# Kernel tuning notes

Measured on AMD Instinct MI355X. Metric: run time of the kernel, lower is better.

The kernel has to match this reference:

```python
import jax, jax.numpy as jnp
import numpy as np

B, T, V, E, H, FC, O = 4096, 64, 512, 32, 128, 256, 1024


def setup_inputs() -> dict:
    key = jax.random.key(0)
    ks = jax.random.split(key, 12)
    n = lambda k, shape, sc=1.0: (jax.random.normal(k, shape, jnp.float32) * sc)
    return {
        "message": n(ks[0], (B, T, V), 0.1),
        "W_emb": n(ks[1], (E, V), 0.05),
        "b_emb": n(ks[2], (E,), 0.05),
        "init_emb": n(ks[3], (1, 1, E), 1.0),
        "W_ih": n(ks[4], (3 * H, E), 0.08),
        "W_hh": n(ks[5], (3 * H, H), 0.08),
        "b_ih": n(ks[6], (3 * H,), 0.05),
        "b_hh": n(ks[7], (3 * H,), 0.05),
        "W_fc1": n(ks[8], (FC, H), 0.08),
        "b_fc1": n(ks[9], (FC,), 0.05),
        "W_fc2": n(ks[10], (O, FC), 0.05),
        "b_fc2": n(ks[11], (O,), 0.05),
    }


def reference(message, W_emb, b_emb, init_emb, W_ih, W_hh, b_ih, b_hh,
              W_fc1, b_fc1, W_fc2, b_fc2):
    Bb, Tt, Vv = message.shape
    Hh = W_hh.shape[1]
    # Per-step embedding of the message (torch does this inside the loop;
    # it is a pure per-timestep linear so we batch it once): [B,T,E]
    emb = jnp.einsum('btv,ev->bte', message, W_emb) + b_emb
    # Inputs consumed by the GRU at step t: initial_embedding at t=0,
    # then embedding(message[:, t-1]) for t >= 1. The embedding of the
    # final token is computed in torch but never fed to the GRU.
    x0 = jnp.broadcast_to(init_emb[0], (Bb, init_emb.shape[-1]))  # [B,E]
    xs = jnp.concatenate([x0[:, None, :], emb[:, :Tt - 1, :]], axis=1)  # [B,T,E]
    # Precompute input-side gate pre-activations for all steps: [T,B,3H]
    gi_all = jnp.einsum('bte,ge->tbg', xs, W_ih) + b_ih

    def gru_step(h, gi):
        gh = h @ W_hh.T + b_hh  # [B,3H]
        i_r, i_z, i_n = jnp.split(gi, 3, axis=-1)
        h_r, h_z, h_n = jnp.split(gh, 3, axis=-1)
        r = jax.nn.sigmoid(i_r + h_r)
        z = jax.nn.sigmoid(i_z + h_z)
        nng = jnp.tanh(i_n + r * h_n)
        h_new = (1.0 - z) * nng + z * h
        return h_new, None

    h0 = jnp.zeros((Bb, Hh), message.dtype)
    h_last, _ = jax.lax.scan(gru_step, h0, gi_all)
    hid = jax.nn.elu(h_last @ W_fc1.T + b_fc1)
    return jax.nn.sigmoid(hid @ W_fc2.T + b_fc2)
```

## Files before the change

### kernel.cpp

```cpp
#include <hip/hip_runtime.h>
#include <math.h>

#define B_ 4096
#define T_ 64
#define V_ 512
#define E_ 32
#define H_ 128
#define FC1_ 256
#define O_ 1024

typedef float f32x4 __attribute__((ext_vector_type(4)));
typedef short s16x8 __attribute__((ext_vector_type(8)));
typedef unsigned short u16;

#define MFMA16(a, b, c) __builtin_amdgcn_mfma_f32_16x16x32_bf16(a, b, c, 0, 0, 0)

#define LDS_BARRIER() do {                                   \
    asm volatile("s_waitcnt lgkmcnt(0)" ::: "memory");       \
    __builtin_amdgcn_s_barrier();                            \
} while (0)

union Frag { u16 q[8]; unsigned u[4]; s16x8 v; };

__device__ __forceinline__ u16 f2bf(float f) {
    union { float f; unsigned u; } v; v.f = f;
    unsigned r = v.u + 0x7FFFu + ((v.u >> 16) & 1u);
    return (u16)(r >> 16);
}
__device__ __forceinline__ unsigned cvtpk(float lo, float hi) {
    unsigned r;
    asm("v_cvt_pk_bf16_f32 %0, %1, %2" : "=v"(r) : "v"(lo), "v"(hi));
    return r;
}
__device__ __forceinline__ float sigf(float x) { return 1.0f / (1.0f + __expf(-x)); }
__device__ __forceinline__ float tanhfast(float x) {
    return 1.0f - 2.0f / (__expf(2.0f * x) + 1.0f);
}

__global__ void __launch_bounds__(256) prep_kernel(
    const float* __restrict__ Wih, const float* __restrict__ Whh,
    const float* __restrict__ Wemb, const float* __restrict__ Wfc1,
    const float* __restrict__ Wfc2,
    u16* __restrict__ wihF, u16* __restrict__ whhF, u16* __restrict__ wembF,
    u16* __restrict__ wfc1F, u16* __restrict__ wfc2F) {
    int id = blockIdx.x * 256 + threadIdx.x;
    int np = gridDim.x * 256;
    for (int i = id; i < 24 * 4 * 64 * 8; i += np) {
        int j = i & 7, l = (i >> 3) & 63, kc = (i >> 9) & 3, gt = i >> 11;
        whhF[i] = f2bf(Whh[(gt * 16 + (l & 15)) * 128 + kc * 32 + (l >> 4) * 8 + j]);
    }
    for (int i = id; i < 24 * 64 * 8; i += np) {
        int j = i & 7, l = (i >> 3) & 63, gt = i >> 9;
        wihF[i] = f2bf(Wih[(gt * 16 + (l & 15)) * 32 + (l >> 4) * 8 + j]);
    }
    for (int i = id; i < 2 * 16 * 64 * 8; i += np) {
        int j = i & 7, l = (i >> 3) & 63, kc = (i >> 9) & 15, nt = i >> 13;
        wembF[i] = f2bf(Wemb[(nt * 16 + (l & 15)) * 512 + kc * 32 + (l >> 4) * 8 + j]);
    }
    for (int i = id; i < 16 * 4 * 64 * 8; i += np) {
        int j = i & 7, l = (i >> 3) & 63, kc = (i >> 9) & 3, ot = i >> 11;
        wfc1F[i] = f2bf(Wfc1[(ot * 16 + (l & 15)) * 128 + kc * 32 + (l >> 4) * 8 + j]);
    }
    for (int i = id; i < 64 * 8 * 64 * 8; i += np) {
        int j = i & 7, l = (i >> 3) & 63, kc = (i >> 9) & 7, nt = i >> 12;
        wfc2F[i] = f2bf(Wfc2[(nt * 16 + (l & 15)) * 256 + kc * 32 + (l >> 4) * 8 + j]);
    }
}

__global__ void __launch_bounds__(512, 2) fused_kernel(
    const float* __restrict__ msg,
    const u16* __restrict__ whhF8, const u16* __restrict__ wihF8,
    const u16* __restrict__ wembF8,
    const float* __restrict__ b_ih, const float* __restrict__ b_hh,
    const float* __restrict__ b_emb, const float* __restrict__ init_emb,
    const u16* __restrict__ wfc1F8, const float* __restrict__ b_fc1,
    const u16* __restrict__ wfc2F8, const float* __restrict__ b_fc2,
    float* __restrict__ out) {
    __shared__ u16 hlds[2][16 * 136];
    __shared__ float epart[2][8][576];
    __shared__ u16 xfrag[2][640];
    __shared__ u16 hidl[16 * 264];
    const int tid = threadIdx.x, w = tid >> 6, l = tid & 63;
    const int ln = l & 15, lh = l >> 4;
    const int wg = w & 3, wp = w >> 2;
    const int gb = blockIdx.x;

    for (int i = tid; i < 16 * 136; i += 512) hlds[0][i] = 0;

    const s16x8* whhFv = (const s16x8*)whhF8;
    const s16x8* wihFv = (const s16x8*)wihF8;
    const s16x8* wembFv = (const s16x8*)wembF8;
    s16x8 wh[3][4], wi[3], we[2][2];
    float br, bz, bin, bgn;
    {
        #pragma unroll
        for (int g = 0; g < 3; g++) {
            int gt = wg + 4 * wp + 8 * g;
            #pragma unroll
            for (int kc = 0; kc < 4; kc++) wh[g][kc] = whhFv[(gt * 4 + kc) * 64 + l];
            wi[g] = wihFv[gt * 64 + l];
        }
        int c = wg * 16 + wp * 64 + ln;
        br  = b_ih[c] + b_hh[c];
        bz  = b_ih[128 + c] + b_hh[128 + c];
        bin = b_ih[256 + c];
        bgn = b_hh[256 + c];
        #pragma unroll
        for (int kk = 0; kk < 2; kk++) {
            we[kk][0] = wembFv[(2 * w + kk) * 64 + l];
            we[kk][1] = wembFv[(16 + 2 * w + kk) * 64 + l];
        }
    }
    const float bev = b_emb[tid & 31];

    s16x8 xinit;
    {
        Frag xi;
        #pragma unroll
        for (int j = 0; j < 8; j++) xi.q[j] = f2bf(init_emb[lh * 8 + j]);
        xinit = xi.v;
    }
    float hold[4] = {};
    const float* mrow = msg + (size_t)(gb * 16 + ln) * T_ * V_ + (2 * w) * 32 + lh * 8;
    f32x4 mb0[4], mb1[4], mb2[4], mb3[4];
#define LOADCOL(BUF, C) do {                                   \
    const float* p_ = mrow + (size_t)(C) * 512;                \
    BUF[0] = *(const f32x4*)(p_);                              \
    BUF[1] = *(const f32x4*)(p_ + 4);                          \
    BUF[2] = *(const f32x4*)(p_ + 32);                         \
    BUF[3] = *(const f32x4*)(p_ + 36);                         \
} while (0)

#define EMBED_STORE(MC, PAR) do {                               \
    f32x4 e0 = {0.f, 0.f, 0.f, 0.f}, e1 = {0.f, 0.f, 0.f, 0.f}; \
    _Pragma("unroll")                                           \
    for (int kk = 0; kk < 2; kk++) {                            \
        Frag fa;                                                \
        fa.u[0] = cvtpk(MC[2 * kk][0], MC[2 * kk][1]);          \
        fa.u[1] = cvtpk(MC[2 * kk][2], MC[2 * kk][3]);          \
        fa.u[2] = cvtpk(MC[2 * kk + 1][0], MC[2 * kk + 1][1]);  \
        fa.u[3] = cvtpk(MC[2 * kk + 1][2], MC[2 * kk + 1][3]);  \
        e0 = MFMA16(fa.v, we[kk][0], e0);                       \
        e1 = MFMA16(fa.v, we[kk][1], e1);                       \
    }                                                           \
    _Pragma("unroll")                                           \
    for (int i = 0; i < 4; i++) {                               \
        epart[PAR][w][(lh * 4 + i) * 36 + ln]      = e0[i];     \
        epart[PAR][w][(lh * 4 + i) * 36 + 16 + ln] = e1[i];     \
    }                                                           \
} while (0)

    LOADCOL(mb3, 0);
    EMBED_STORE(mb3, 1);
    LOADCOL(mb0, 1); LOADCOL(mb1, 2); LOADCOL(mb2, 3);
    LDS_BARRIER();

    const int aoff = ln * 136 + lh * 8;
    const int colo = wg * 16 + wp * 64 + ln;
    const int fr = tid >> 5, fc = tid & 31, fo = fr * 36 + fc;

#define GRU_STEP(TT, MC, MN) do {                                              \
    const int t = (TT);                                                        \
    if (t <= 58) LOADCOL(MN, t + 4);                                           \
    const u16* hb = hlds[t & 1];                                               \
    s16x8 af0 = *(const s16x8*)(hb + aoff);                                    \
    s16x8 af1 = *(const s16x8*)(hb + aoff + 32);                               \
    s16x8 af2 = *(const s16x8*)(hb + aoff + 64);                               \
    s16x8 af3 = *(const s16x8*)(hb + aoff + 96);                               \
    s16x8 xc;                                                                  \
    if (t == 0) xc = xinit;                                                    \
    else xc = *(const s16x8*)(&xfrag[(t + 1) & 1][0] + ln * 40 + lh * 8);      \
    f32x4 ar  = {br, br, br, br};                                              \
    f32x4 az  = {bz, bz, bz, bz};                                              \
    f32x4 agn = {bgn, bgn, bgn, bgn};                                          \
    f32x4 ain = {bin, bin, bin, bin};                                          \
    ar  = MFMA16(xc, wi[0], ar);                                               \
    az  = MFMA16(xc, wi[1], az);                                               \
    ain = MFMA16(xc, wi[2], ain);                                              \
    ar  = MFMA16(af0, wh[0][0], ar);                                           \
    ar  = MFMA16(af1, wh[0][1], ar);                                           \
    ar  = MFMA16(af2, wh[0][2], ar);                                           \
    ar  = MFMA16(af3, wh[0][3], ar);                                           \
    az  = MFMA16(af0, wh[1][0], az);                                           \
    az  = MFMA16(af1, wh[1][1], az);                                           \
    az  = MFMA16(af2, wh[1][2], az);                                           \
    az  = MFMA16(af3, wh[1][3], az);                                           \
    agn = MFMA16(af0, wh[2][0], agn);                                          \
    agn = MFMA16(af1, wh[2][1], agn);                                          \
    agn = MFMA16(af2, wh[2][2], agn);                                          \
    agn = MFMA16(af3, wh[2][3], agn);                                          \
    u16* hw = hlds[(t + 1) & 1];                                               \
    float hn[4];                                                               \
    _Pragma("unroll")                                                          \
    for (int i = 0; i < 4; i++) {                                              \
        float rg = sigf(ar[i]);                                                \
        float zg = sigf(az[i]);                                                \
        float ng = tanhfast(ain[i] + rg * agn[i]);                             \
        hn[i] = zg * (hold[i] - ng) + ng;                                      \
        hold[i] = hn[i];                                                       \
    }                                                                          \
    {                                                                          \
        unsigned u01 = cvtpk(hn[0], hn[1]);                                    \
        unsigned u23 = cvtpk(hn[2], hn[3]);                                    \
        hw[(lh * 4 + 0) * 136 + colo] = (u16)(u01 & 0xFFFFu);                  \
        hw[(lh * 4 + 1) * 136 + colo] = (u16)(u01 >> 16);                      \
        hw[(lh * 4 + 2) * 136 + colo] = (u16)(u23 & 0xFFFFu);                  \
        hw[(lh * 4 + 3) * 136 + colo] = (u16)(u23 >> 16);                      \
    }                                                                          \
    if (t <= 61) EMBED_STORE(MC, t & 1);                                       \
    if (t <= 62) {                                                             \
        const float* eb = &epart[(t + 1) & 1][0][0];                           \
        float s = eb[fo]            + eb[576 + fo]     + eb[2 * 576 + fo]      \
                + eb[3 * 576 + fo]  + eb[4 * 576 + fo] + eb[5 * 576 + fo]      \
                + eb[6 * 576 + fo]  + eb[7 * 576 + fo] + bev;                  \
        xfrag[t & 1][fr * 40 + fc] = f2bf(s);                                  \
    }                                                                          \
    LDS_BARRIER();                                                             \
} while (0)

    for (int tt = 0; tt < 64; tt += 4) {
        GRU_STEP(tt + 0, mb0, mb3);
        GRU_STEP(tt + 1, mb1, mb0);
        GRU_STEP(tt + 2, mb2, mb1);
        GRU_STEP(tt + 3, mb3, mb2);
    }
#undef GRU_STEP
#undef LOADCOL
#undef EMBED_STORE

    const u16* hb = hlds[0];
    s16x8 hf0 = *(const s16x8*)(hb + aoff);
    s16x8 hf1 = *(const s16x8*)(hb + aoff + 32);
    s16x8 hf2 = *(const s16x8*)(hb + aoff + 64);
    s16x8 hf3 = *(const s16x8*)(hb + aoff + 96);
    const s16x8* w1v = (const s16x8*)wfc1F8;
    #pragma unroll
    for (int q = 0; q < 2; q++) {
        int ot = 2 * w + q;
        float b1 = b_fc1[ot * 16 + ln];
        f32x4 a1 = {b1, b1, b1, b1};
        a1 = MFMA16(hf0, w1v[(ot * 4 + 0) * 64 + l], a1);
        a1 = MFMA16(hf1, w1v[(ot * 4 + 1) * 64 + l], a1);
        a1 = MFMA16(hf2, w1v[(ot * 4 + 2) * 64 + l], a1);
        a1 = MFMA16(hf3, w1v[(ot * 4 + 3) * 64 + l], a1);
        #pragma unroll
        for (int i = 0; i < 4; i++) {
            float v = a1[i];
            v = v > 0.0f ? v : (__expf(v) - 1.0f);
            hidl[(lh * 4 + i) * 264 + ot * 16 + ln] = f2bf(v);
        }
    }
    LDS_BARRIER();

    s16x8 hf[8];
    #pragma unroll
    for (int kc = 0; kc < 8; kc++)
        hf[kc] = *(const s16x8*)(hidl + ln * 264 + kc * 32 + lh * 8);
    const s16x8* w2v = (const s16x8*)wfc2F8;
    #pragma unroll
    for (int q = 0; q < 8; q++) {
        int nt = 8 * w + q;
        float b2 = b_fc2[nt * 16 + ln];
        f32x4 a2 = {b2, b2, b2, b2};
        #pragma unroll
        for (int kc = 0; kc < 8; kc++)
            a2 = MFMA16(hf[kc], w2v[(nt * 8 + kc) * 64 + l], a2);
        #pragma unroll
        for (int i = 0; i < 4; i++)
            out[(size_t)(gb * 16 + lh * 4 + i) * 1024 + nt * 16 + ln] = sigf(a2[i]);
    }
}

extern "C" void kernel_launch(void* const* d_in, const int* in_sizes, int n_in,
                              void* d_out, int out_size, void* d_ws, size_t ws_size,
                              hipStream_t stream) {
    const float* message  = (const float*)d_in[0];
    const float* W_emb    = (const float*)d_in[1];
    const float* b_emb    = (const float*)d_in[2];
    const float* init_emb = (const float*)d_in[3];
    const float* W_ih     = (const float*)d_in[4];
    const float* W_hh     = (const float*)d_in[5];
    const float* b_ih     = (const float*)d_in[6];
    const float* b_hh     = (const float*)d_in[7];
    const float* W_fc1    = (const float*)d_in[8];
    const float* b_fc1    = (const float*)d_in[9];
    const float* W_fc2    = (const float*)d_in[10];
    const float* b_fc2    = (const float*)d_in[11];
    float* out = (float*)d_out;

    u16* whhF  = (u16*)d_ws;
    u16* wihF  = whhF  + 49152;
    u16* wembF = wihF  + 12288;
    u16* wfc1F = wembF + 16384;
    u16* wfc2F = wfc1F + 32768;

    hipLaunchKernelGGL(prep_kernel, dim3(256), dim3(256), 0, stream,
                       W_ih, W_hh, W_emb, W_fc1, W_fc2, wihF, whhF, wembF, wfc1F, wfc2F);
    hipLaunchKernelGGL(fused_kernel, dim3(256), dim3(512), 0, stream,
                       message, whhF, wihF, wembF, b_ih, b_hh, b_emb, init_emb,
                       wfc1F, b_fc1, wfc2F, b_fc2, out);
}
```

Baseline: 132.2 us.

## Drop weight prep kernel and stream message tiles via global_load_lds

Removes the separate prep kernel that repacked the weights into bf16 fragment layouts. The fused kernel now gathers and converts fp32 weights directly from global memory. Message columns are no longer prefetched into registers four steps ahead; they are double-buffered in LDS with asynchronous global_load_lds, two steps ahead. This saves a kernel launch and frees registers, at the cost of more LDS (about 66KB extra for mlds, which may limit occupancy at 2 blocks/CU), uncoalesced fp32 weight loads in the fc2 epilogue, and a shorter prefetch distance.

Measured after the change: 158.1 us. 1.2x slower.

```diff
diff --git a/kernel.cpp b/kernel.cpp
--- a/kernel.cpp
+++ b/kernel.cpp
@@ -15,11 +15,6 @@
 
 #define MFMA16(a, b, c) __builtin_amdgcn_mfma_f32_16x16x32_bf16(a, b, c, 0, 0, 0)
 
-#define LDS_BARRIER() do {                                   \
-    asm volatile("s_waitcnt lgkmcnt(0)" ::: "memory");       \
-    __builtin_amdgcn_s_barrier();                            \
-} while (0)
-
 union Frag { u16 q[8]; unsigned u[4]; s16x8 v; };
 
 __device__ __forceinline__ u16 f2bf(float f) {
@@ -36,46 +31,32 @@
 __device__ __forceinline__ float tanhfast(float x) {
     return 1.0f - 2.0f / (__expf(2.0f * x) + 1.0f);
 }
-
-__global__ void __launch_bounds__(256) prep_kernel(
-    const float* __restrict__ Wih, const float* __restrict__ Whh,
-    const float* __restrict__ Wemb, const float* __restrict__ Wfc1,
-    const float* __restrict__ Wfc2,
-    u16* __restrict__ wihF, u16* __restrict__ whhF, u16* __restrict__ wembF,
-    u16* __restrict__ wfc1F, u16* __restrict__ wfc2F) {
-    int id = blockIdx.x * 256 + threadIdx.x;
-    int np = gridDim.x * 256;
-    for (int i = id; i < 24 * 4 * 64 * 8; i += np) {
-        int j = i & 7, l = (i >> 3) & 63, kc = (i >> 9) & 3, gt = i >> 11;
-        whhF[i] = f2bf(Whh[(gt * 16 + (l & 15)) * 128 + kc * 32 + (l >> 4) * 8 + j]);
-    }
-    for (int i = id; i < 24 * 64 * 8; i += np) {
-        int j = i & 7, l = (i >> 3) & 63, gt = i >> 9;
-        wihF[i] = f2bf(Wih[(gt * 16 + (l & 15)) * 32 + (l >> 4) * 8 + j]);
-    }
-    for (int i = id; i < 2 * 16 * 64 * 8; i += np) {
-        int j = i & 7, l = (i >> 3) & 63, kc = (i >> 9) & 15, nt = i >> 13;
-        wembF[i] = f2bf(Wemb[(nt * 16 + (l & 15)) * 512 + kc * 32 + (l >> 4) * 8 + j]);
-    }
-    for (int i = id; i < 16 * 4 * 64 * 8; i += np) {
-        int j = i & 7, l = (i >> 3) & 63, kc = (i >> 9) & 3, ot = i >> 11;
-        wfc1F[i] = f2bf(Wfc1[(ot * 16 + (l & 15)) * 128 + kc * 32 + (l >> 4) * 8 + j]);
-    }
-    for (int i = id; i < 64 * 8 * 64 * 8; i += np) {
-        int j = i & 7, l = (i >> 3) & 63, kc = (i >> 9) & 7, nt = i >> 12;
-        wfc2F[i] = f2bf(Wfc2[(nt * 16 + (l & 15)) * 256 + kc * 32 + (l >> 4) * 8 + j]);
-    }
+__device__ __forceinline__ void gll16(const float* gsrc, float* ldst) {
+    __builtin_amdgcn_global_load_lds(
+        (const __attribute__((address_space(1))) unsigned int*)gsrc,
+        (__attribute__((address_space(3))) unsigned int*)ldst,
+        16, 0, 0);
+}
+__device__ __forceinline__ s16x8 gatherB(const float* W, int row, int K, int k0, int lh) {
+    const float* p = W + (size_t)row * K + k0 + lh * 8;
+    float4 a = *(const float4*)p;
+    float4 b = *(const float4*)(p + 4);
+    Frag f;
+    f.u[0] = cvtpk(a.x, a.y); f.u[1] = cvtpk(a.z, a.w);
+    f.u[2] = cvtpk(b.x, b.y); f.u[3] = cvtpk(b.z, b.w);
+    return f.v;
 }
 
 __global__ void __launch_bounds__(512, 2) fused_kernel(
     const float* __restrict__ msg,
-    const u16* __restrict__ whhF8, const u16* __restrict__ wihF8,
-    const u16* __restrict__ wembF8,
+    const float* __restrict__ Wemb, const float* __restrict__ b_emb,
+    const float* __restrict__ init_emb,
+    const float* __restrict__ Wih, const float* __restrict__ Whh,
     const float* __restrict__ b_ih, const float* __restrict__ b_hh,
-    const float* __restrict__ b_emb, const float* __restrict__ init_emb,
-    const u16* __restrict__ wfc1F8, const float* __restrict__ b_fc1,
-    const u16* __restrict__ wfc2F8, const float* __restrict__ b_fc2,
+    const float* __restrict__ Wfc1, const float* __restrict__ b_fc1,
+    const float* __restrict__ Wfc2, const float* __restrict__ b_fc2,
     float* __restrict__ out) {
+    __shared__ float mlds[2][16][516];
     __shared__ u16 hlds[2][16 * 136];
     __shared__ float epart[2][8][576];
     __shared__ u16 xfrag[2][640];
@@ -87,9 +68,19 @@
 
     for (int i = tid; i < 16 * 136; i += 512) hlds[0][i] = 0;
 
-    const s16x8* whhFv = (const s16x8*)whhF8;
-    const s16x8* wihFv = (const s16x8*)wihF8;
-    const s16x8* wembFv = (const s16x8*)wembF8;
+#define GLL_COL(C, BUF) do {                                                   \
+    _Pragma("unroll")                                                          \
+    for (int i_ = 0; i_ < 4; i_++) {                                           \
+        int r_ = 2 * w + (i_ >> 1);                                            \
+        int h_ = (i_ & 1) * 256;                                               \
+        gll16(msg + ((size_t)(gb * 16 + r_) * T_ + (C)) * V_ + h_ + l * 4,     \
+              &mlds[BUF][r_][h_]);                                             \
+    }                                                                          \
+} while (0)
+
+    GLL_COL(0, 0);
+    GLL_COL(1, 1);
+
     s16x8 wh[3][4], wi[3], we[2][2];
     float br, bz, bin, bgn;
     {
@@ -97,22 +88,22 @@
         for (int g = 0; g < 3; g++) {
             int gt = wg + 4 * wp + 8 * g;
             #pragma unroll
-            for (int kc = 0; kc < 4; kc++) wh[g][kc] = whhFv[(gt * 4 + kc) * 64 + l];
-            wi[g] = wihFv[gt * 64 + l];
+            for (int kc = 0; kc < 4; kc++)
+                wh[g][kc] = gatherB(Whh, gt * 16 + ln, 128, kc * 32, lh);
+            wi[g] = gatherB(Wih, gt * 16 + ln, 32, 0, lh);
+        }
+        #pragma unroll
+        for (int kk = 0; kk < 2; kk++) {
+            we[kk][0] = gatherB(Wemb, ln, 512, (2 * w + kk) * 32, lh);
+            we[kk][1] = gatherB(Wemb, 16 + ln, 512, (2 * w + kk) * 32, lh);
         }
         int c = wg * 16 + wp * 64 + ln;
         br  = b_ih[c] + b_hh[c];
         bz  = b_ih[128 + c] + b_hh[128 + c];
         bin = b_ih[256 + c];
         bgn = b_hh[256 + c];
-        #pragma unroll
-        for (int kk = 0; kk < 2; kk++) {
-            we[kk][0] = wembFv[(2 * w + kk) * 64 + l];
-            we[kk][1] = wembFv[(16 + 2 * w + kk) * 64 + l];
-        }
     }
     const float bev = b_emb[tid & 31];
-
     s16x8 xinit;
     {
         Frag xi;
@@ -121,47 +112,38 @@
         xinit = xi.v;
     }
     float hold[4] = {};
-    const float* mrow = msg + (size_t)(gb * 16 + ln) * T_ * V_ + (2 * w) * 32 + lh * 8;
-    f32x4 mb0[4], mb1[4], mb2[4], mb3[4];
-#define LOADCOL(BUF, C) do {                                   \
-    const float* p_ = mrow + (size_t)(C) * 512;                \
-    BUF[0] = *(const f32x4*)(p_);                              \
-    BUF[1] = *(const f32x4*)(p_ + 4);                          \
-    BUF[2] = *(const f32x4*)(p_ + 32);                         \
-    BUF[3] = *(const f32x4*)(p_ + 36);                         \
+    __syncthreads();
+
+#define EMBED_LDS(BUF, PAR) do {                                               \
+    f32x4 e0 = {0.f, 0.f, 0.f, 0.f}, e1 = {0.f, 0.f, 0.f, 0.f};                \
+    _Pragma("unroll")                                                          \
+    for (int kk = 0; kk < 2; kk++) {                                           \
+        const float* mp = &mlds[BUF][ln][(2 * w + kk) * 32 + lh * 8];          \
+        f32x4 m0 = *(const f32x4*)mp;                                          \
+        f32x4 m1 = *(const f32x4*)(mp + 4);                                    \
+        Frag fa;                                                               \
+        fa.u[0] = cvtpk(m0[0], m0[1]); fa.u[1] = cvtpk(m0[2], m0[3]);          \
+        fa.u[2] = cvtpk(m1[0], m1[1]); fa.u[3] = cvtpk(m1[2], m1[3]);          \
+        e0 = MFMA16(fa.v, we[kk][0], e0);                                      \
+        e1 = MFMA16(fa.v, we[kk][1], e1);                                      \
+    }                                                                          \
+    _Pragma("unroll")                                                          \
+    for (int i = 0; i < 4; i++) {                                              \
+        epart[PAR][w][(lh * 4 + i) * 36 + ln]      = e0[i];                    \
+        epart[PAR][w][(lh * 4 + i) * 36 + 16 + ln] = e1[i];                    \
+    }                                                                          \
 } while (0)
 
-#define EMBED_STORE(MC, PAR) do {                               \
-    f32x4 e0 = {0.f, 0.f, 0.f, 0.f}, e1 = {0.f, 0.f, 0.f, 0.f}; \
-    _Pragma("unroll")                                           \
-    for (int kk = 0; kk < 2; kk++) {                            \
-        Frag fa;                                                \
-        fa.u[0] = cvtpk(MC[2 * kk][0], MC[2 * kk][1]);          \
-        fa.u[1] = cvtpk(MC[2 * kk][2], MC[2 * kk][3]);          \
-        fa.u[2] = cvtpk(MC[2 * kk + 1][0], MC[2 * kk + 1][1]);  \
-        fa.u[3] = cvtpk(MC[2 * kk + 1][2], MC[2 * kk + 1][3]);  \
-        e0 = MFMA16(fa.v, we[kk][0], e0);                       \
-        e1 = MFMA16(fa.v, we[kk][1], e1);                       \
-    }                                                           \
-    _Pragma("unroll")                                           \
-    for (int i = 0; i < 4; i++) {                               \
-        epart[PAR][w][(lh * 4 + i) * 36 + ln]      = e0[i];     \
-        epart[PAR][w][(lh * 4 + i) * 36 + 16 + ln] = e1[i];     \
-    }                                                           \
-} while (0)
-
-    LOADCOL(mb3, 0);
-    EMBED_STORE(mb3, 1);
-    LOADCOL(mb0, 1); LOADCOL(mb1, 2); LOADCOL(mb2, 3);
-    LDS_BARRIER();
+    EMBED_LDS(0, 1);
+    __syncthreads();
 
     const int aoff = ln * 136 + lh * 8;
     const int colo = wg * 16 + wp * 64 + ln;
     const int fr = tid >> 5, fc = tid & 31, fo = fr * 36 + fc;
 
-#define GRU_STEP(TT, MC, MN) do {                                              \
+#define GRU_STEP(TT) do {                                                      \
     const int t = (TT);                                                        \
-    if (t <= 58) LOADCOL(MN, t + 4);                                           \
+    if (t <= 60) GLL_COL(t + 2, t & 1);                                        \
     const u16* hb = hlds[t & 1];                                               \
     s16x8 af0 = *(const s16x8*)(hb + aoff);                                    \
     s16x8 af1 = *(const s16x8*)(hb + aoff + 32);                               \
@@ -207,42 +189,39 @@
         hw[(lh * 4 + 2) * 136 + colo] = (u16)(u23 & 0xFFFFu);                  \
         hw[(lh * 4 + 3) * 136 + colo] = (u16)(u23 >> 16);                      \
     }                                                                          \
-    if (t <= 61) EMBED_STORE(MC, t & 1);                                       \
+    if (t <= 61) EMBED_LDS((t + 1) & 1, t & 1);                                \
     if (t <= 62) {                                                             \
         const float* eb = &epart[(t + 1) & 1][0][0];                           \
-        float s = eb[fo]            + eb[576 + fo]     + eb[2 * 576 + fo]      \
-                + eb[3 * 576 + fo]  + eb[4 * 576 + fo] + eb[5 * 576 + fo]      \
-                + eb[6 * 576 + fo]  + eb[7 * 576 + fo] + bev;                  \
+        float s = eb[fo]           + eb[576 + fo]     + eb[2 * 576 + fo]       \
+                + eb[3 * 576 + fo] + eb[4 * 576 + fo] + eb[5 * 576 + fo]       \
+                + eb[6 * 576 + fo] + eb[7 * 576 + fo] + bev;                   \
         xfrag[t & 1][fr * 40 + fc] = f2bf(s);                                  \
     }                                                                          \
-    LDS_BARRIER();                                                             \
+    __syncthreads();                                                           \
 } while (0)
 
-    for (int tt = 0; tt < 64; tt += 4) {
-        GRU_STEP(tt + 0, mb0, mb3);
-        GRU_STEP(tt + 1, mb1, mb0);
-        GRU_STEP(tt + 2, mb2, mb1);
-        GRU_STEP(tt + 3, mb3, mb2);
+    for (int tt = 0; tt < 64; tt += 2) {
+        GRU_STEP(tt);
+        GRU_STEP(tt + 1);
     }
 #undef GRU_STEP
-#undef LOADCOL
-#undef EMBED_STORE
+#undef GLL_COL
+#undef EMBED_LDS
 
     const u16* hb = hlds[0];
     s16x8 hf0 = *(const s16x8*)(hb + aoff);
     s16x8 hf1 = *(const s16x8*)(hb + aoff + 32);
     s16x8 hf2 = *(const s16x8*)(hb + aoff + 64);
     s16x8 hf3 = *(const s16x8*)(hb + aoff + 96);
-    const s16x8* w1v = (const s16x8*)wfc1F8;
     #pragma unroll
     for (int q = 0; q < 2; q++) {
         int ot = 2 * w + q;
         float b1 = b_fc1[ot * 16 + ln];
         f32x4 a1 = {b1, b1, b1, b1};
-        a1 = MFMA16(hf0, w1v[(ot * 4 + 0) * 64 + l], a1);
-        a1 = MFMA16(hf1, w1v[(ot * 4 + 1) * 64 + l], a1);
-        a1 = MFMA16(hf2, w1v[(ot * 4 + 2) * 64 + l], a1);
-        a1 = MFMA16(hf3, w1v[(ot * 4 + 3) * 64 + l], a1);
+        a1 = MFMA16(hf0, gatherB(Wfc1, ot * 16 + ln, 128, 0,  lh), a1);
+        a1 = MFMA16(hf1, gatherB(Wfc1, ot * 16 + ln, 128, 32, lh), a1);
+        a1 = MFMA16(hf2, gatherB(Wfc1, ot * 16 + ln, 128, 64, lh), a1);
+        a1 = MFMA16(hf3, gatherB(Wfc1, ot * 16 + ln, 128, 96, lh), a1);
         #pragma unroll
         for (int i = 0; i < 4; i++) {
             float v = a1[i];
@@ -250,13 +229,12 @@
             hidl[(lh * 4 + i) * 264 + ot * 16 + ln] = f2bf(v);
         }
     }
-    LDS_BARRIER();
+    __syncthreads();
 
     s16x8 hf[8];
     #pragma unroll
     for (int kc = 0; kc < 8; kc++)
         hf[kc] = *(const s16x8*)(hidl + ln * 264 + kc * 32 + lh * 8);
-    const s16x8* w2v = (const s16x8*)wfc2F8;
     #pragma unroll
     for (int q = 0; q < 8; q++) {
         int nt = 8 * w + q;
@@ -264,7 +242,7 @@
         f32x4 a2 = {b2, b2, b2, b2};
         #pragma unroll
         for (int kc = 0; kc < 8; kc++)
-            a2 = MFMA16(hf[kc], w2v[(nt * 8 + kc) * 64 + l], a2);
+            a2 = MFMA16(hf[kc], gatherB(Wfc2, nt * 16 + ln, 256, kc * 32, lh), a2);
         #pragma unroll
         for (int i = 0; i < 4; i++)
             out[(size_t)(gb * 16 + lh * 4 + i) * 1024 + nt * 16 + ln] = sigf(a2[i]);
@@ -287,16 +265,9 @@
     const float* W_fc2    = (const float*)d_in[10];
     const float* b_fc2    = (const float*)d_in[11];
     float* out = (float*)d_out;
-
-    u16* whhF  = (u16*)d_ws;
-    u16* wihF  = whhF  + 49152;
-    u16* wembF = wihF  + 12288;
-    u16* wfc1F = wembF + 16384;
-    u16* wfc2F = wfc1F + 32768;
-
-    hipLaunchKernelGGL(prep_kernel, dim3(256), dim3(256), 0, stream,
-                       W_ih, W_hh, W_emb, W_fc1, W_fc2, wihF, whhF, wembF, wfc1F, wfc2F);
+    (void)d_ws; (void)ws_size;
+
     hipLaunchKernelGGL(fused_kernel, dim3(256), dim3(512), 0, stream,
-                       message, whhF, wihF, wembF, b_ih, b_hh, b_emb, init_emb,
-                       wfc1F, b_fc1, wfc2F, b_fc2, out);
-}
+                       message, W_emb, b_emb, init_emb, W_ih, W_hh, b_ih, b_hh,
+                       W_fc1, b_fc1, W_fc2, b_fc2, out);
+}
```
